# Kernel tuning notes

Hardware: AMD Instinct MI355X
Metric: run time of the kernel (lower is better)

## Reference

```python
import jax, jax.numpy as jnp
import numpy as np

ALPHA = 0.5
GAMMA = 0.001
BIG = 1e10  # stand-in for +inf on DP borders (DILATE uses 1e10 in dtw_grad)

B, L, DIM = 32, 512, 16


def softdtw_single(D, gamma):
    """Soft-DTW value for one [N,N] cost matrix via anti-diagonal wavefront.
    Padded grid Rp[(N+1),(N+1)]: Rp[0,0]=0, borders=BIG,
    Rp[i,j] = D[i-1,j-1] + softmin_gamma(Rp[i-1,j], Rp[i-1,j-1], Rp[i,j-1]).
    Returns Rp[N,N]."""
    N = D.shape[0]
    ii = jnp.arange(N + 1)
    diag0 = jnp.full((N + 1,), BIG, D.dtype).at[0].set(0.0)  # diagonal d=0
    diag1 = jnp.full((N + 1,), BIG, D.dtype)                 # diagonal d=1 (borders)

    def step(carry, d):
        prev2, prev1 = carry  # diagonals d-2, d-1; prev1[i] = Rp[i, d-1-i]
        j = d - ii
        valid = (ii >= 1) & (ii <= N) & (j >= 1) & (j <= N)
        dval = D[jnp.clip(ii - 1, 0, N - 1), jnp.clip(j - 1, 0, N - 1)]
        a = jnp.roll(prev1, 1).at[0].set(BIG)  # Rp[i-1, j]
        b = jnp.roll(prev2, 1).at[0].set(BIG)  # Rp[i-1, j-1]
        c = prev1                               # Rp[i, j-1]
        sm = -gamma * jax.nn.logsumexp(jnp.stack([a, b, c]) * (-1.0 / gamma), axis=0)
        cur = jnp.where(valid, dval + sm, BIG)
        return (prev1, cur), None

    (_, last), _ = jax.lax.scan(step, (diag0, diag1), jnp.arange(2, 2 * N + 1))
    return last[N]


def batched_sq_dists(x, y):
    # dist[b,i,j] = clamp(||x[b,i]-y[b,j]||^2, 0)
    xn = jnp.sum(x * x, -1)[:, :, None]
    yn = jnp.sum(y * y, -1)[:, None, :]
    return jnp.clip(xn + yn - 2.0 * jnp.einsum('bid,bjd->bij', x, y), 0.0)


def dilate_loss(inp, tgt):
    # base=None path: shift input so its first step is at the origin
    x = inp - inp[:, 0:1, :]
    D = batched_sq_dists(tgt, x)  # D[b] = pairwise_distances(target[b], input[b])
    # SoftDTW value and soft alignment path (= grad of value wrt D, as in DILATE PathDTW)
    vals, paths = jax.vmap(jax.value_and_grad(lambda Dk: softdtw_single(Dk, GAMMA)))(D)
    loss_shape = jnp.mean(vals)
    N = D.shape[1]
    idx = jnp.arange(N, dtype=D.dtype)
    Omega = (idx[:, None] - idx[None, :]) ** 2  # pairwise sq dists of arange(N)
    path = jnp.mean(paths, axis=0)
    loss_temporal = jnp.sum(path * Omega) / (N * N)
    return ALPHA * loss_shape + (1.0 - ALPHA) * loss_temporal


def setup_inputs() -> dict:
    key = jax.random.key(0)
    k1, k2 = jax.random.split(key)
    inp = jax.random.normal(k1, (B, L, DIM), dtype=jnp.float32)
    tgt = jax.random.normal(k2, (B, L, DIM), dtype=jnp.float32)
    return {"input": inp, "target": tgt}


def reference(input, target):
    return dilate_loss(input, target)
```

## Files before the change

### kernel.cpp

```cpp
#include <hip/hip_runtime.h>
#include <stdint.h>


#define N 512
#define NB 32
#define BIGF 1e10f
#define QN 512
#define STRF2 ((size_t)QN * 1024)
#define VOMAX2 ((int)(STRF2 * 4 - 16))

typedef unsigned int u32;
typedef float f32x4 __attribute__((ext_vector_type(4)));
typedef float f32x2 __attribute__((ext_vector_type(2)));

__device__ __forceinline__ float dppshr(float x, float oldv) {
    return __int_as_float(__builtin_amdgcn_update_dpp(
        __float_as_int(oldv), __float_as_int(x), 0x138, 0xF, 0xF, false));
}

__global__ __launch_bounds__(512) void kA(const float* __restrict__ inp,
                                          const float* __restrict__ tgt,
                                          float* __restrict__ Dg) {
    const int b = blockIdx.y;
    const int jc = blockIdx.x;
    const int tid = (int)threadIdx.x;
    __shared__ float xs[4][16];
    if (tid < 64) {
        int c = tid >> 4, d = tid & 15;
        int j = jc * 4 + c;
        xs[c][d] = inp[(((size_t)b * N + j) << 4) + d] -
                   inp[(((size_t)b * N) << 4) + d];
    }
    __syncthreads();
    const float4* t4 = (const float4*)(tgt + (((size_t)b * N + tid) << 4));
    float4 ta = t4[0], tb = t4[1], tc = t4[2], td = t4[3];
    float s[4];
#pragma unroll
    for (int c = 0; c < 4; ++c) {
        float acc = 0.f, e;
        e = ta.x - xs[c][0];  acc = fmaf(e, e, acc);
        e = ta.y - xs[c][1];  acc = fmaf(e, e, acc);
        e = ta.z - xs[c][2];  acc = fmaf(e, e, acc);
        e = ta.w - xs[c][3];  acc = fmaf(e, e, acc);
        e = tb.x - xs[c][4];  acc = fmaf(e, e, acc);
        e = tb.y - xs[c][5];  acc = fmaf(e, e, acc);
        e = tb.z - xs[c][6];  acc = fmaf(e, e, acc);
        e = tb.w - xs[c][7];  acc = fmaf(e, e, acc);
        e = tc.x - xs[c][8];  acc = fmaf(e, e, acc);
        e = tc.y - xs[c][9];  acc = fmaf(e, e, acc);
        e = tc.z - xs[c][10]; acc = fmaf(e, e, acc);
        e = tc.w - xs[c][11]; acc = fmaf(e, e, acc);
        e = td.x - xs[c][12]; acc = fmaf(e, e, acc);
        e = td.y - xs[c][13]; acc = fmaf(e, e, acc);
        e = td.z - xs[c][14]; acc = fmaf(e, e, acc);
        e = td.w - xs[c][15]; acc = fmaf(e, e, acc);
        s[c] = acc;
    }
    float* outB = Dg + (size_t)b * STRF2;
    const int q0 = jc * 2 + (tid >> 1);
    f32x2 w0; w0.x = s[0]; w0.y = s[1];
    f32x2 w1; w1.x = s[2]; w1.y = s[3];
    *(f32x2*)(outB + (size_t)q0 * 1024 + tid * 2) = w0;
    *(f32x2*)(outB + (size_t)(q0 + 1) * 1024 + tid * 2) = w1;
}

__global__ __launch_bounds__(256) void kP(const float* __restrict__ Dg,
                                          float* __restrict__ acc) {
    const int b = blockIdx.x;
    const int tid = (int)threadIdx.x;
    const int w = tid >> 6, lam = tid & 63;
    const float* __restrict__ Db = Dg + (size_t)b * STRF2;

    __shared__ __align__(16) f32x2 ring[3][64];
    __shared__ __align__(16) f32x2 dump2[72];

    for (int i = tid; i < 3 * 64 + 72; i += 256) {
        f32x2 z; z.x = BIGF; z.y = 0.f;
        ((f32x2*)ring)[i] = z;
    }
    __syncthreads();

    int vo0, vo1, vo2, vo3, vo4, vo5, vo6, vo7;
    f32x4 d0, d1, d2, d3, d4, d5, d6, d7;
    {
        const int vb = tid * 16 - 16 * w * 4096;
        vo0 = vb;            vo1 = vb + 4096;     vo2 = vb + 2 * 4096;
        vo3 = vb + 3 * 4096; vo4 = vb + 4 * 4096; vo5 = vb + 5 * 4096;
        vo6 = vb + 6 * 4096; vo7 = vb + 7 * 4096;
    }

#define LOAD(k)                                                               \
    do {                                                                      \
        int va_ = min(max(vo##k, 0), VOMAX2);                                 \
        asm volatile("global_load_dwordx4 %0, %1, %2"                         \
                     : "=v"(d##k) : "v"(va_), "s"(Db));                       \
    } while (0)

    LOAD(0); LOAD(1); LOAD(2); LOAD(3); LOAD(4); LOAD(5); LOAD(6); LOAD(7);

    float L0R = BIGF, L1R = BIGF, L0T = 0.f, L1T = 0.f;
    float hA = BIGF, hB = BIGF, hAT = 0.f, hBT = 0.f;
    float sBold = (tid == 0) ? 0.f : BIGF, sBoldT = 0.f;
    float dr = (float)(4 * tid + 32 * w);
    int pp = -(tid + 16 * w);
    float Rfin = 0.f, Tfin = 0.f;

    const bool is_cons = (lam == 0) && (w > 0);
    f32x2* base2 = ((lam == 63) && (w < 3)) ? &ring[w][0] : &dump2[0];
    const f32x2* ringR = (w > 0) ? &ring[w - 1][0] : &ring[0][0];
    int rb = (-160 * w) & 63;

    f32x4 bkA[4], bkB[4];

#define READBANK(X)                                                           \
    do {                                                                      \
        if (is_cons) {                                                        \
            X[0] = *(const f32x4*)(ringR + (rb & 63));                        \
            X[1] = *(const f32x4*)(ringR + ((rb + 2) & 63));                  \
            X[2] = *(const f32x4*)(ringR + ((rb + 4) & 63));                  \
            X[3] = *(const f32x4*)(ringR + ((rb + 6) & 63));                  \
        }                                                                     \
        rb = (rb + 8) & 63;                                                   \
    } while (0)

    READBANK(bkA);

#define STEP(k, BX, j)                                                        \
    do {                                                                      \
        asm volatile("s_waitcnt vmcnt(7)" : "+v"(d##k));                      \
        float D00 = fmaxf(d##k.x, 0.f), D01 = fmaxf(d##k.y, 0.f);             \
        float D10 = fmaxf(d##k.z, 0.f), D11 = fmaxf(d##k.w, 0.f);             \
        float upA = is_cons ? BX[j].x : hA;                                   \
        float utA = is_cons ? BX[j].y : hAT;                                  \
        float upB = is_cons ? BX[j].z : hB;                                   \
        float utB = is_cons ? BX[j].w : hBT;                                  \
                                          \
        float mn0 = fminf(upA, fminf(sBold, L0R));                            \
        float Ts0 = (mn0 == sBold) ? sBoldT : ((mn0 == upA) ? utA : L0T);     \
        float R00 = D00 + mn0;                                                \
        float T00 = fmaf(dr, dr, Ts0);                                        \
                                             \
        float mn1 = fminf(R00, fminf(L0R, L1R));                              \
        float Ts1 = (mn1 == L0R) ? L0T : ((mn1 == R00) ? T00 : L1T);          \
        float drp = dr + 1.f;                                                 \
        float R10 = D10 + mn1;                                                \
        float T10 = fmaf(drp, drp, Ts1);                                      \
                                           \
        float mn2 = fminf(upB, fminf(upA, R00));                              \
        float Ts2 = (mn2 == upA) ? utA : ((mn2 == upB) ? utB : T00);          \
        float drm = dr - 1.f;                                                 \
        float R01 = D01 + mn2;                                                \
        float T01 = fmaf(drm, drm, Ts2);                                      \
                                           \
        float mn3 = fminf(R01, fminf(R00, R10));                              \
        float Ts3 = (mn3 == R00) ? T00 : ((mn3 == R01) ? T01 : T10);          \
        float R11v = D11 + mn3;                                               \
        float T11v = fmaf(dr, dr, Ts3);                                       \
        bool hit = (pp == 255);                                               \
        Rfin = hit ? R11v : Rfin;                                             \
        Tfin = hit ? T11v : Tfin;                                             \
        {                                                                     \
            int c0_ = 2 * pp;                                                 \
            f32x4 wv; wv.x = R10; wv.y = T10; wv.z = R11v; wv.w = T11v;       \
            *(f32x4*)(base2 + (c0_ & 63)) = wv;                               \
        }                                                                     \
        L0R = R01; L0T = T01; L1R = R11v; L1T = T11v;                         \
        sBold = upB; sBoldT = utB;                                            \
        hA = dppshr(R10, BIGF); hAT = dppshr(T10, 0.f);                       \
        hB = dppshr(R11v, BIGF); hBT = dppshr(T11v, 0.f);                     \
        dr -= 2.f; pp += 1;                                                   \
        vo##k += 32768;             \
        LOAD(k);                                                              \
    } while (0)

    for (int n = 0; n < 70; ++n) {
        asm volatile("s_waitcnt lgkmcnt(0)" ::: "memory");
        __builtin_amdgcn_s_barrier();
        READBANK(bkB);
        STEP(0, bkA, 0); STEP(1, bkA, 1); STEP(2, bkA, 2); STEP(3, bkA, 3);
        READBANK(bkA);
        STEP(4, bkB, 0); STEP(5, bkB, 1); STEP(6, bkB, 2); STEP(7, bkB, 3);
    }
#undef STEP
#undef READBANK
#undef LOAD

    asm volatile("s_waitcnt vmcnt(0)" ::: "memory");
    if (tid == 255) {
        acc[b] = Rfin;
        acc[NB + b] = Tfin;
    }
}

__global__ void kC(const float* __restrict__ acc, float* __restrict__ out) {
    const int l = (int)threadIdx.x;
    float vs = (l < NB) ? acc[l] : 0.f;
    float vt = (l < NB) ? acc[NB + l] : 0.f;
#pragma unroll
    for (int o = 32; o >= 1; o >>= 1) {
        vs += __shfl_down(vs, o);
        vt += __shfl_down(vt, o);
    }
    if (l == 0)
        out[0] = 0.5f * (vs / (float)NB) +
                 0.5f * (vt / ((float)NB * (float)(N * N)));
}

__global__ void kSentinel(float* out) { out[0] = -12345.0f; }

extern "C" void kernel_launch(void* const* d_in, const int* in_sizes, int n_in,
                              void* d_out, int out_size, void* d_ws, size_t ws_size,
                              hipStream_t stream) {
    const float* inp = (const float*)d_in[0];
    const float* tgt = (const float*)d_in[1];
    float* out = (float*)d_out;

    const size_t DSZ = (size_t)NB * STRF2 * sizeof(float);
    const size_t NEEDED = 256 + DSZ;
    if (ws_size < NEEDED) {
        kSentinel<<<1, 1, 0, stream>>>(out);
        return;
    }
    char* ws = (char*)d_ws;
    float* acc = (float*)ws;
    float* Dg = (float*)(ws + 256);

    kA<<<dim3(N / 4, NB), 512, 0, stream>>>(inp, tgt, Dg);
    kP<<<NB, 256, 0, stream>>>(Dg, acc);
    kC<<<1, 64, 0, stream>>>(acc, out);
}
```

Measured before the change: 106.1 us.

## Pack two batch wavefront DPs into one 512-thread workgroup

The soft-DTW wavefront kernel now runs two batch elements per workgroup, 16 blocks of 512 threads instead of 32 blocks of 256. Each half gets its own LDS ring, and global loads use a per-batch byte offset from a shared base pointer. The aim is to put two independent latency-bound recurrences on one CU so each SIMD can interleave two waves and hide load and dependency stalls. In exchange, both halves now share every block-wide barrier and half as many CUs are used.

```diff
diff --git a/kernel.cpp b/kernel.cpp
--- a/kernel.cpp
+++ b/kernel.cpp
@@ -64,17 +64,19 @@
     *(f32x2*)(outB + (size_t)(q0 + 1) * 1024 + tid * 2) = w1;
 }
 
-__global__ __launch_bounds__(256) void kP(const float* __restrict__ Dg,
+__global__ __launch_bounds__(512) void kP(const float* __restrict__ Dg,
                                           float* __restrict__ acc) {
-    const int b = blockIdx.x;
     const int tid = (int)threadIdx.x;
-    const int w = tid >> 6, lam = tid & 63;
-    const float* __restrict__ Db = Dg + (size_t)b * STRF2;
-
-    __shared__ __align__(16) f32x2 ring[3][64];
+    const int h = tid >> 8;
+    const int tp = tid & 255;
+    const int w = tp >> 6, lam = tp & 63;
+    const int b = blockIdx.x * 2 + h;
+    const int bOff = (int)((size_t)b * STRF2 * 4);
+
+    __shared__ __align__(16) f32x2 ring[2][3][64];
     __shared__ __align__(16) f32x2 dump2[72];
 
-    for (int i = tid; i < 3 * 64 + 72; i += 256) {
+    for (int i = tid; i < 2 * 3 * 64 + 72; i += 512) {
         f32x2 z; z.x = BIGF; z.y = 0.f;
         ((f32x2*)ring)[i] = z;
     }
@@ -83,7 +85,7 @@
     int vo0, vo1, vo2, vo3, vo4, vo5, vo6, vo7;
     f32x4 d0, d1, d2, d3, d4, d5, d6, d7;
     {
-        const int vb = tid * 16 - 16 * w * 4096;
+        const int vb = tp * 16 - 16 * w * 4096;
         vo0 = vb;            vo1 = vb + 4096;     vo2 = vb + 2 * 4096;
         vo3 = vb + 3 * 4096; vo4 = vb + 4 * 4096; vo5 = vb + 5 * 4096;
         vo6 = vb + 6 * 4096; vo7 = vb + 7 * 4096;
@@ -91,23 +93,23 @@
 
 #define LOAD(k)                                                               \
     do {                                                                      \
-        int va_ = min(max(vo##k, 0), VOMAX2);                                 \
+        int va_ = min(max(vo##k, 0), VOMAX2) + bOff;                          \
         asm volatile("global_load_dwordx4 %0, %1, %2"                         \
-                     : "=v"(d##k) : "v"(va_), "s"(Db));                       \
+                     : "=v"(d##k) : "v"(va_), "s"(Dg));                       \
     } while (0)
 
     LOAD(0); LOAD(1); LOAD(2); LOAD(3); LOAD(4); LOAD(5); LOAD(6); LOAD(7);
 
     float L0R = BIGF, L1R = BIGF, L0T = 0.f, L1T = 0.f;
     float hA = BIGF, hB = BIGF, hAT = 0.f, hBT = 0.f;
-    float sBold = (tid == 0) ? 0.f : BIGF, sBoldT = 0.f;
-    float dr = (float)(4 * tid + 32 * w);
-    int pp = -(tid + 16 * w);
+    float sBold = (tp == 0) ? 0.f : BIGF, sBoldT = 0.f;
+    float dr = (float)(4 * tp + 32 * w);
+    int pp = -(tp + 16 * w);
     float Rfin = 0.f, Tfin = 0.f;
 
     const bool is_cons = (lam == 0) && (w > 0);
-    f32x2* base2 = ((lam == 63) && (w < 3)) ? &ring[w][0] : &dump2[0];
-    const f32x2* ringR = (w > 0) ? &ring[w - 1][0] : &ring[0][0];
+    f32x2* base2 = ((lam == 63) && (w < 3)) ? &ring[h][w][0] : &dump2[0];
+    const f32x2* ringR = (w > 0) ? &ring[h][w - 1][0] : &ring[h][0][0];
     int rb = (-160 * w) & 63;
 
     f32x4 bkA[4], bkB[4];
@@ -186,7 +188,7 @@
 #undef LOAD
 
     asm volatile("s_waitcnt vmcnt(0)" ::: "memory");
-    if (tid == 255) {
+    if (tp == 255) {
         acc[b] = Rfin;
         acc[NB + b] = Tfin;
     }
@@ -226,6 +228,6 @@
     float* Dg = (float*)(ws + 256);
 
     kA<<<dim3(N / 4, NB), 512, 0, stream>>>(inp, tgt, Dg);
-    kP<<<NB, 256, 0, stream>>>(Dg, acc);
+    kP<<<NB / 2, 512, 0, stream>>>(Dg, acc);
     kC<<<1, 64, 0, stream>>>(acc, out);
 }
```

Result: slower. 148.7 us (+40.2%).

## Restructure distance kernel into skewed stores and prefetch ring values per step

Applied to the files above, without the earlier changes.

The distance kernel now stages all 512 shifted input rows in shared memory per block and loops over 64 skewed rows per block, writing only valid entries. This replaces the 128-block grid, which re-read and re-shifted the input for every column chunk. In the DP kernel, the 8-wide ring bank reads are replaced by a 2-deep rolling prefetch issued inside each step, which cuts register pressure. The risk is that the wait on the LDS load now falls closer to where the value is used, and the distance kernel runs only 256 blocks with a serial loop.

```diff
diff --git a/kernel.cpp b/kernel.cpp
--- a/kernel.cpp
+++ b/kernel.cpp
@@ -22,46 +22,62 @@
                                           const float* __restrict__ tgt,
                                           float* __restrict__ Dg) {
     const int b = blockIdx.y;
-    const int jc = blockIdx.x;
+    const int qbase = blockIdx.x * 64;
     const int tid = (int)threadIdx.x;
-    __shared__ float xs[4][16];
-    if (tid < 64) {
-        int c = tid >> 4, d = tid & 15;
-        int j = jc * 4 + c;
-        xs[c][d] = inp[(((size_t)b * N + j) << 4) + d] -
-                   inp[(((size_t)b * N) << 4) + d];
+    __shared__ float xls[512 * 20];
+
+    {
+        const float4* ip = (const float4*)(inp + (((size_t)b * N + tid) << 4));
+        const float4* op = (const float4*)(inp + (((size_t)b * N) << 4));
+        float4 v0 = ip[0], v1 = ip[1], v2 = ip[2], v3 = ip[3];
+        float4 o0 = op[0], o1 = op[1], o2 = op[2], o3 = op[3];
+        v0.x -= o0.x; v0.y -= o0.y; v0.z -= o0.z; v0.w -= o0.w;
+        v1.x -= o1.x; v1.y -= o1.y; v1.z -= o1.z; v1.w -= o1.w;
+        v2.x -= o2.x; v2.y -= o2.y; v2.z -= o2.z; v2.w -= o2.w;
+        v3.x -= o3.x; v3.y -= o3.y; v3.z -= o3.z; v3.w -= o3.w;
+        float* xr = xls + tid * 20;
+        ((float4*)xr)[0] = v0; ((float4*)(xr + 4))[0] = v1;
+        ((float4*)(xr + 8))[0] = v2; ((float4*)(xr + 12))[0] = v3;
     }
     __syncthreads();
+
     const float4* t4 = (const float4*)(tgt + (((size_t)b * N + tid) << 4));
     float4 ta = t4[0], tb = t4[1], tc = t4[2], td = t4[3];
-    float s[4];
-#pragma unroll
-    for (int c = 0; c < 4; ++c) {
-        float acc = 0.f, e;
-        e = ta.x - xs[c][0];  acc = fmaf(e, e, acc);
-        e = ta.y - xs[c][1];  acc = fmaf(e, e, acc);
-        e = ta.z - xs[c][2];  acc = fmaf(e, e, acc);
-        e = ta.w - xs[c][3];  acc = fmaf(e, e, acc);
-        e = tb.x - xs[c][4];  acc = fmaf(e, e, acc);
-        e = tb.y - xs[c][5];  acc = fmaf(e, e, acc);
-        e = tb.z - xs[c][6];  acc = fmaf(e, e, acc);
-        e = tb.w - xs[c][7];  acc = fmaf(e, e, acc);
-        e = tc.x - xs[c][8];  acc = fmaf(e, e, acc);
-        e = tc.y - xs[c][9];  acc = fmaf(e, e, acc);
-        e = tc.z - xs[c][10]; acc = fmaf(e, e, acc);
-        e = tc.w - xs[c][11]; acc = fmaf(e, e, acc);
-        e = td.x - xs[c][12]; acc = fmaf(e, e, acc);
-        e = td.y - xs[c][13]; acc = fmaf(e, e, acc);
-        e = td.z - xs[c][14]; acc = fmaf(e, e, acc);
-        e = td.w - xs[c][15]; acc = fmaf(e, e, acc);
-        s[c] = acc;
-    }
     float* outB = Dg + (size_t)b * STRF2;
-    const int q0 = jc * 2 + (tid >> 1);
-    f32x2 w0; w0.x = s[0]; w0.y = s[1];
-    f32x2 w1; w1.x = s[2]; w1.y = s[3];
-    *(f32x2*)(outB + (size_t)q0 * 1024 + tid * 2) = w0;
-    *(f32x2*)(outB + (size_t)(q0 + 1) * 1024 + tid * 2) = w1;
+
+    for (int qi = 0; qi < 64; ++qi) {
+        const int q = qbase + qi;
+        const int g = q - (tid >> 1);
+        const bool valid = (unsigned)g <= 255u;
+        const int j = min(max(g, 0), 255) * 2;
+        const float* xr = xls + j * 20;
+        const float* xs = xr + 20;
+        float4 xa = ((const float4*)xr)[0], xb = ((const float4*)(xr + 4))[0];
+        float4 xc = ((const float4*)(xr + 8))[0], xd = ((const float4*)(xr + 12))[0];
+        float4 ya = ((const float4*)xs)[0], yb = ((const float4*)(xs + 4))[0];
+        float4 yc = ((const float4*)(xs + 8))[0], yd = ((const float4*)(xs + 12))[0];
+        float sA = 0.f, sB = 0.f, e;
+        e = ta.x - xa.x; sA = fmaf(e, e, sA);  e = ta.x - ya.x; sB = fmaf(e, e, sB);
+        e = ta.y - xa.y; sA = fmaf(e, e, sA);  e = ta.y - ya.y; sB = fmaf(e, e, sB);
+        e = ta.z - xa.z; sA = fmaf(e, e, sA);  e = ta.z - ya.z; sB = fmaf(e, e, sB);
+        e = ta.w - xa.w; sA = fmaf(e, e, sA);  e = ta.w - ya.w; sB = fmaf(e, e, sB);
+        e = tb.x - xb.x; sA = fmaf(e, e, sA);  e = tb.x - yb.x; sB = fmaf(e, e, sB);
+        e = tb.y - xb.y; sA = fmaf(e, e, sA);  e = tb.y - yb.y; sB = fmaf(e, e, sB);
+        e = tb.z - xb.z; sA = fmaf(e, e, sA);  e = tb.z - yb.z; sB = fmaf(e, e, sB);
+        e = tb.w - xb.w; sA = fmaf(e, e, sA);  e = tb.w - yb.w; sB = fmaf(e, e, sB);
+        e = tc.x - xc.x; sA = fmaf(e, e, sA);  e = tc.x - yc.x; sB = fmaf(e, e, sB);
+        e = tc.y - xc.y; sA = fmaf(e, e, sA);  e = tc.y - yc.y; sB = fmaf(e, e, sB);
+        e = tc.z - xc.z; sA = fmaf(e, e, sA);  e = tc.z - yc.z; sB = fmaf(e, e, sB);
+        e = tc.w - xc.w; sA = fmaf(e, e, sA);  e = tc.w - yc.w; sB = fmaf(e, e, sB);
+        e = td.x - xd.x; sA = fmaf(e, e, sA);  e = td.x - yd.x; sB = fmaf(e, e, sB);
+        e = td.y - xd.y; sA = fmaf(e, e, sA);  e = td.y - yd.y; sB = fmaf(e, e, sB);
+        e = td.z - xd.z; sA = fmaf(e, e, sA);  e = td.z - yd.z; sB = fmaf(e, e, sB);
+        e = td.w - xd.w; sA = fmaf(e, e, sA);  e = td.w - yd.w; sB = fmaf(e, e, sB);
+        if (valid) {
+            f32x2 wv; wv.x = sA; wv.y = sB;
+            *(f32x2*)(outB + (size_t)q * 1024 + tid * 2) = wv;
+        }
+    }
 }
 
 __global__ __launch_bounds__(256) void kP(const float* __restrict__ Dg,
@@ -110,30 +126,24 @@
     const f32x2* ringR = (w > 0) ? &ring[w - 1][0] : &ring[0][0];
     int rb = (-160 * w) & 63;
 
-    f32x4 bkA[4], bkB[4];
-
-#define READBANK(X)                                                           \
-    do {                                                                      \
-        if (is_cons) {                                                        \
-            X[0] = *(const f32x4*)(ringR + (rb & 63));                        \
-            X[1] = *(const f32x4*)(ringR + ((rb + 2) & 63));                  \
-            X[2] = *(const f32x4*)(ringR + ((rb + 4) & 63));                  \
-            X[3] = *(const f32x4*)(ringR + ((rb + 6) & 63));                  \
-        }                                                                     \
-        rb = (rb + 8) & 63;                                                   \
-    } while (0)
-
-    READBANK(bkA);
-
-#define STEP(k, BX, j)                                                        \
+    f32x4 pf0, pf1;
+    pf0.x = BIGF; pf0.y = 0.f; pf0.z = BIGF; pf0.w = 0.f;
+    pf1 = pf0;
+    if (is_cons) {
+        pf0 = *(const f32x4*)(ringR + rb);
+        pf1 = *(const f32x4*)(ringR + ((rb + 2) & 63));
+    }
+    rb = (rb + 4) & 63;
+
+#define STEP(k, PF)                                                           \
     do {                                                                      \
         asm volatile("s_waitcnt vmcnt(7)" : "+v"(d##k));                      \
         float D00 = fmaxf(d##k.x, 0.f), D01 = fmaxf(d##k.y, 0.f);             \
         float D10 = fmaxf(d##k.z, 0.f), D11 = fmaxf(d##k.w, 0.f);             \
-        float upA = is_cons ? BX[j].x : hA;                                   \
-        float utA = is_cons ? BX[j].y : hAT;                                  \
-        float upB = is_cons ? BX[j].z : hB;                                   \
-        float utB = is_cons ? BX[j].w : hBT;                                  \
+        float upA = is_cons ? PF.x : hA;                                      \
+        float utA = is_cons ? PF.y : hAT;                                     \
+        float upB = is_cons ? PF.z : hB;                                      \
+        float utB = is_cons ? PF.w : hBT;                                     \
                                           \
         float mn0 = fminf(upA, fminf(sBold, L0R));                            \
         float Ts0 = (mn0 == sBold) ? sBoldT : ((mn0 == upA) ? utA : L0T);     \
@@ -168,6 +178,8 @@
         sBold = upB; sBoldT = utB;                                            \
         hA = dppshr(R10, BIGF); hAT = dppshr(T10, 0.f);                       \
         hB = dppshr(R11v, BIGF); hBT = dppshr(T11v, 0.f);                     \
+        if (is_cons) { PF = *(const f32x4*)(ringR + rb); }                    \
+        rb = (rb + 2) & 63;                                                   \
         dr -= 2.f; pp += 1;                                                   \
         vo##k += 32768;             \
         LOAD(k);                                                              \
@@ -176,13 +188,10 @@
     for (int n = 0; n < 70; ++n) {
         asm volatile("s_waitcnt lgkmcnt(0)" ::: "memory");
         __builtin_amdgcn_s_barrier();
-        READBANK(bkB);
-        STEP(0, bkA, 0); STEP(1, bkA, 1); STEP(2, bkA, 2); STEP(3, bkA, 3);
-        READBANK(bkA);
-        STEP(4, bkB, 0); STEP(5, bkB, 1); STEP(6, bkB, 2); STEP(7, bkB, 3);
+        STEP(0, pf0); STEP(1, pf1); STEP(2, pf0); STEP(3, pf1);
+        STEP(4, pf0); STEP(5, pf1); STEP(6, pf0); STEP(7, pf1);
     }
 #undef STEP
-#undef READBANK
 #undef LOAD
 
     asm volatile("s_waitcnt vmcnt(0)" ::: "memory");
@@ -225,7 +234,7 @@
     float* acc = (float*)ws;
     float* Dg = (float*)(ws + 256);
 
-    kA<<<dim3(N / 4, NB), 512, 0, stream>>>(inp, tgt, Dg);
+    kA<<<dim3(8, NB), 512, 0, stream>>>(inp, tgt, Dg);
     kP<<<NB, 256, 0, stream>>>(Dg, acc);
     kC<<<1, 64, 0, stream>>>(acc, out);
 }
```

Measured after the change: 120.3 us. 13.4% more time.
